# Performance work log

Hardware: AMD Instinct MI355X
Metric: run time of the kernel (lower is better)

The kernel has to match this reference:

```python
import jax, jax.numpy as jnp
import numpy as np

D_MODEL = 1024
N_HEADS = 16
HEAD_DIM = D_MODEL // N_HEADS
BLOCK_SIZE = 2048
B, T = 4, 2048


def setup_inputs() -> dict:
    key = jax.random.key(0)
    ks = jax.random.split(key, 5)
    s = 0.02
    x = jax.random.normal(ks[0], (B, T, D_MODEL), dtype=jnp.float32)
    W_qkv = jax.random.normal(ks[1], (D_MODEL, 3 * D_MODEL), dtype=jnp.float32) * s
    b_qkv = jnp.zeros((3 * D_MODEL,), dtype=jnp.float32)
    W_proj = jax.random.normal(ks[2], (D_MODEL, D_MODEL), dtype=jnp.float32) * s
    b_proj = jnp.zeros((D_MODEL,), dtype=jnp.float32)
    return {"x": x, "W_qkv": W_qkv, "b_qkv": b_qkv, "W_proj": W_proj, "b_proj": b_proj}


def reference(x, W_qkv, b_qkv, W_proj, b_proj):
    Bsz, Tlen, C = x.shape
    qkv = x @ W_qkv + b_qkv                      # [B,T,3C]
    q, k, v = jnp.split(qkv, 3, axis=2)
    # [B,T,C] -> [B,H,T,hd]
    def heads(t):
        return t.reshape(Bsz, Tlen, N_HEADS, HEAD_DIM).transpose(0, 2, 1, 3)
    q, k, v = heads(q), heads(k), heads(v)
    scale = 1.0 / jnp.sqrt(jnp.asarray(HEAD_DIM, dtype=x.dtype))
    att = jnp.einsum('bhqd,bhkd->bhqk', q, k) * scale   # [B,H,T,T]
    causal = jnp.tril(jnp.ones((Tlen, Tlen), dtype=bool))
    att = jnp.where(causal, att, jnp.asarray(-jnp.inf, dtype=att.dtype))
    att = jax.nn.softmax(att, axis=-1)
    y = jnp.einsum('bhqk,bhkd->bhqd', att, v)            # [B,H,T,hd]
    y = y.transpose(0, 2, 1, 3).reshape(Bsz, Tlen, C)
    return y @ W_proj + b_proj
```

## Files before the change

### kernel.cpp

```cpp
#include <hip/hip_runtime.h>
#include <hip/hip_bf16.h>

#define D_MODEL 1024
#define N_HEADS 16
#define HEAD_DIM 64
#define SEQ_T 2048
#define BATCH 4

#define SL2E 0.18033688011f

typedef short s8v  __attribute__((ext_vector_type(8)));
typedef float f32x4 __attribute__((ext_vector_type(4)));
typedef unsigned long long ull;

static __device__ __forceinline__ unsigned short f2bf(float f) {
  union { float f; unsigned int u; } v; v.f = f;
  unsigned int u = v.u;
  return (unsigned short)((u + 0x7FFF + ((u >> 16) & 1)) >> 16);
}

static __device__ __forceinline__ unsigned int cvtpk_bf16(float lo, float hi) {
  unsigned int r;
  asm("v_cvt_pk_bf16_f32 %0, %1, %2" : "=v"(r) : "v"(lo), "v"(hi));
  return r;
}

#if __has_builtin(__builtin_amdgcn_exp2f)
#define EXP2(x) __builtin_amdgcn_exp2f(x)
#else
#define EXP2(x) exp2f(x)
#endif

static __device__ __forceinline__ void glds16(const void* g, void* l) {
  __builtin_amdgcn_global_load_lds(
      (const __attribute__((address_space(1))) void*)g,
      (__attribute__((address_space(3))) void*)l, 16, 0, 0);
}

template<int MODE>
__global__ __launch_bounds__(256) void gemm_bt_kernel(
    const unsigned short* __restrict__ A, const unsigned short* __restrict__ Bt,
    const float* __restrict__ bias, float* __restrict__ Cout,
    unsigned short* __restrict__ qkb, unsigned short* __restrict__ vT,
    int M, int N, int K)
{
  __shared__ unsigned short Al[128 * 64];
  __shared__ unsigned short Bl[128 * 64];

  const int tid  = threadIdx.x;
  const int lane = tid & 63;
  const int wave = tid >> 6;
  const int col  = lane & 15;
  const int quad = lane >> 4;
  const int wm   = (wave & 1) * 64;
  const int wn   = (wave >> 1) * 64;
  const int bm0  = blockIdx.y * 128;
  const int bn0  = blockIdx.x * 128;
  const int cx   = col & 7;

  f32x4 acc[4][4];
  #pragma unroll
  for (int t = 0; t < 4; ++t)
    #pragma unroll
    for (int u = 0; u < 4; ++u) acc[t][u] = (f32x4)0.f;

  for (int k0 = 0; k0 < K; k0 += 64) {
    __syncthreads();
    #pragma unroll
    for (int i = 0; i < 4; ++i) {
      int idx = i * 256 + tid;
      int row = idx >> 3;
      int gc  = (idx & 7) ^ (row & 7);
      glds16(A  + (size_t)(bm0 + row) * K + k0 + gc * 8, &Al[idx * 8]);
      glds16(Bt + (size_t)(bn0 + row) * K + k0 + gc * 8, &Bl[idx * 8]);
    }
    __syncthreads();

    #pragma unroll
    for (int s = 0; s < 2; ++s) {
      s8v af[4], bf[4];
      #pragma unroll
      for (int t = 0; t < 4; ++t) {
        int ar = wm + t * 16 + col;
        af[t] = *(const s8v*)&Al[ar * 64 + (((s * 4 + quad) ^ cx) * 8)];
        int br = wn + t * 16 + col;
        bf[t] = *(const s8v*)&Bl[br * 64 + (((s * 4 + quad) ^ cx) * 8)];
      }
      #pragma unroll
      for (int t = 0; t < 4; ++t)
        #pragma unroll
        for (int u = 0; u < 4; ++u)
          acc[t][u] = __builtin_amdgcn_mfma_f32_16x16x32_bf16(
              af[t], bf[u], acc[t][u], 0, 0, 0);
    }
  }

  float bv[4];
  #pragma unroll
  for (int u = 0; u < 4; ++u) bv[u] = bias[bn0 + wn + u * 16 + col];

  if (MODE == 1 && bn0 >= 2048) {
    #pragma unroll
    for (int t = 0; t < 4; ++t) {
      int m_base = bm0 + wm + t * 16 + quad * 4;
      #pragma unroll
      for (int u = 0; u < 4; ++u) {
        int hd = (bn0 + wn + u * 16 + col) - 2048;
        size_t bh = (size_t)(bm0 >> 11) * 16 + (hd >> 6);
        ull pk = (ull)f2bf(acc[t][u][0] + bv[u])
               | ((ull)f2bf(acc[t][u][1] + bv[u]) << 16)
               | ((ull)f2bf(acc[t][u][2] + bv[u]) << 32)
               | ((ull)f2bf(acc[t][u][3] + bv[u]) << 48);
        *(ull*)(vT + (bh * 64 + (hd & 63)) * 2048 + (m_base & 2047)) = pk;
      }
    }
  } else {
    const float sc = (MODE == 1 && (bn0 + wn) < 1024) ? SL2E : 1.0f;
    #pragma unroll
    for (int t = 0; t < 4; ++t) {
      #pragma unroll
      for (int r = 0; r < 4; ++r) {
        size_t m = bm0 + wm + t * 16 + quad * 4 + r;
        #pragma unroll
        for (int u = 0; u < 4; ++u) {
          int n = bn0 + wn + u * 16 + col;
          float v = acc[t][u][r] + bv[u];
          if (MODE == 0) Cout[m * N + n] = v;
          else           qkb[m * 2048 + n] = f2bf(v * sc);
        }
      }
    }
  }
}

static __device__ __forceinline__ void transpose_tile(
    const float* __restrict__ W, unsigned short* __restrict__ Wt,
    int K, int N, int n0, int k0)
{
  __shared__ float tile[32][33];
  const int tx = threadIdx.x & 31, ty = threadIdx.x >> 5;
  #pragma unroll
  for (int i = 0; i < 4; ++i)
    tile[ty + i * 8][tx] = W[(size_t)(k0 + ty + i * 8) * N + n0 + tx];
  __syncthreads();
  #pragma unroll
  for (int i = 0; i < 4; ++i)
    Wt[(size_t)(n0 + ty + i * 8) * K + k0 + tx] = f2bf(tile[tx][ty + i * 8]);
}

__global__ __launch_bounds__(256) void prep_kernel(
    const float* __restrict__ x, const float* __restrict__ W_qkv,
    const float* __restrict__ W_proj, ushort4* __restrict__ xb,
    unsigned short* __restrict__ wqt, unsigned short* __restrict__ wpt)
{
  const int bid = blockIdx.x;
  if (bid < 8192) {
    int i = bid * 256 + threadIdx.x;
    float4 v = ((const float4*)x)[i];
    ushort4 o;
    o.x = f2bf(v.x); o.y = f2bf(v.y); o.z = f2bf(v.z); o.w = f2bf(v.w);
    xb[i] = o;
  } else if (bid < 8192 + 3072) {
    int b2 = bid - 8192;
    transpose_tile(W_qkv, wqt, 1024, 3072, (b2 % 96) * 32, (b2 / 96) * 32);
  } else {
    int b3 = bid - 11264;
    transpose_tile(W_proj, wpt, 1024, 1024, (b3 % 32) * 32, (b3 / 32) * 32);
  }
}

#define LPAD 72

__global__ __launch_bounds__(512, 4) void attn_mfma_kernel(
    const unsigned short* __restrict__ qk, const unsigned short* __restrict__ vT,
    unsigned short* __restrict__ y)
{
  __shared__ unsigned short Ks[2][64 * 64];
  __shared__ unsigned short Vs[2][64 * 64];
  __shared__ unsigned short Ps[256][LPAD];

  const int tid  = threadIdx.x;
  const int wave = tid >> 6;
  const int lane = tid & 63;
  const int col  = lane & 15;
  const int quad = lane >> 4;
  const int cx   = col & 7;

  const int bh = blockIdx.x;
  const int b = bh >> 4, h = bh & 15;
  const int yy = (int)blockIdx.y;
  const int qblk = (yy < 4) ? (7 - yy) : (yy - 4);
  const int q0 = qblk * 256;
  const int nk = 4 * qblk + 4;
  const int C2 = 2048;

  const unsigned short* qbase = qk + (size_t)b * SEQ_T * C2 + h * 64;
  const unsigned short* kbase = qbase + 1024;
  const unsigned short* vbase = vT + (size_t)bh * 64 * 2048;

  s8v qf[2][2];
  #pragma unroll
  for (int s = 0; s < 2; ++s)
    #pragma unroll
    for (int c = 0; c < 2; ++c)
      qf[s][c] = *(const s8v*)(qbase +
          (size_t)(q0 + s * 128 + wave * 16 + col) * C2 + c * 32 + quad * 8);

  f32x4 acc[2][4];
  #pragma unroll
  for (int s = 0; s < 2; ++s)
    #pragma unroll
    for (int t = 0; t < 4; ++t) acc[s][t] = (f32x4)0.f;
  float lsum[2] = {0.f, 0.f};

  auto stage = [&](int kt, int bi) {
    const int k0 = kt * 64;
    int row = tid >> 3;
    int gc  = (tid & 7) ^ (row & 7);
    glds16(kbase + (size_t)(k0 + row) * C2 + gc * 8, &Ks[bi][tid * 8]);
    glds16(vbase + (size_t)row * 2048 + k0 + gc * 8, &Vs[bi][tid * 8]);
  };

  auto tile_body = [&](int kt, int bi) {
    const int k0 = kt * 64;

    s8v kf[4][2];
    #pragma unroll
    for (int t = 0; t < 4; ++t)
      #pragma unroll
      for (int c = 0; c < 2; ++c)
        kf[t][c] = *(const s8v*)&Ks[bi][(t * 16 + col) * 64 + (((c * 4 + quad) ^ cx) * 8)];

    #pragma unroll
    for (int s = 0; s < 2; ++s) {
      const int qs = q0 + s * 128 + wave * 16;
      if (k0 > qs + 15) continue;

      f32x4 st[4];
      #pragma unroll
      for (int t = 0; t < 4; ++t) st[t] = (f32x4)0.f;
      #pragma unroll
      for (int t = 0; t < 4; ++t)
        #pragma unroll
        for (int c = 0; c < 2; ++c)
          st[t] = __builtin_amdgcn_mfma_f32_16x16x32_bf16(kf[t][c], qf[s][c], st[t], 0, 0, 0);

      const bool diag = (k0 + 63 > qs);
      if (!diag) {
        #pragma unroll
        for (int t = 0; t < 4; ++t) {
          float e0 = EXP2(st[t][0]);
          float e1 = EXP2(st[t][1]);
          float e2 = EXP2(st[t][2]);
          float e3 = EXP2(st[t][3]);
          lsum[s] += (e0 + e1) + (e2 + e3);
          uint2 pk;
          pk.x = cvtpk_bf16(e0, e1);
          pk.y = cvtpk_bf16(e2, e3);
          *(uint2*)&Ps[s * 128 + wave * 16 + col][t * 16 + quad * 4] = pk;
        }
      } else {
        const int qg = qs + col;
        #pragma unroll
        for (int t = 0; t < 4; ++t) {
          uint2 pk;
          if (k0 + t * 16 > qs + 15) {
            pk.x = 0u; pk.y = 0u;
          } else {
            float e[4];
            #pragma unroll
            for (int r = 0; r < 4; ++r) {
              float v = EXP2(st[t][r]);
              if (k0 + t * 16 + quad * 4 + r > qg) v = 0.f;
              e[r] = v;
            }
            lsum[s] += (e[0] + e[1]) + (e[2] + e[3]);
            pk.x = cvtpk_bf16(e[0], e[1]);
            pk.y = cvtpk_bf16(e[2], e[3]);
          }
          *(uint2*)&Ps[s * 128 + wave * 16 + col][t * 16 + quad * 4] = pk;
        }
      }
    }

    s8v vf[4][2];
    #pragma unroll
    for (int t = 0; t < 4; ++t)
      #pragma unroll
      for (int c = 0; c < 2; ++c)
        vf[t][c] = *(const s8v*)&Vs[bi][(t * 16 + col) * 64 + (((c * 4 + quad) ^ cx) * 8)];
    #pragma unroll
    for (int s = 0; s < 2; ++s) {
      const int qs = q0 + s * 128 + wave * 16;
      if (k0 > qs + 15) continue;
      s8v pf[2];
      #pragma unroll
      for (int c = 0; c < 2; ++c)
        pf[c] = *(const s8v*)&Ps[s * 128 + wave * 16 + col][c * 32 + quad * 8];
      #pragma unroll
      for (int t = 0; t < 4; ++t)
        #pragma unroll
        for (int c = 0; c < 2; ++c)
          acc[s][t] = __builtin_amdgcn_mfma_f32_16x16x32_bf16(pf[c], vf[t][c], acc[s][t], 0, 0, 0);
    }
  };

  stage(0, 0);
  for (int kt = 0; kt < nk; kt += 2) {
    __syncthreads();
    if (kt + 1 < nk) stage(kt + 1, 1);
    tile_body(kt, 0);
    if (kt + 1 < nk) {
      __syncthreads();
      if (kt + 2 < nk) stage(kt + 2, 0);
      tile_body(kt + 1, 1);
    }
  }

  #pragma unroll
  for (int s = 0; s < 2; ++s) {
    float v = lsum[s];
    v += __shfl_xor(v, 16);
    v += __shfl_xor(v, 32);
    #pragma unroll
    for (int r = 0; r < 4; ++r) {
      float inv = 1.0f / __shfl(v, quad * 4 + r);
      int q = q0 + s * 128 + wave * 16 + quad * 4 + r;
      unsigned short* yrow = y + (size_t)(b * SEQ_T + q) * D_MODEL + h * 64;
      #pragma unroll
      for (int t = 0; t < 4; ++t)
        yrow[t * 16 + col] = f2bf(acc[s][t][r] * inv);
    }
  }
}

extern "C" void kernel_launch(void* const* d_in, const int* in_sizes, int n_in,
                              void* d_out, int out_size, void* d_ws, size_t ws_size,
                              hipStream_t stream) {
  const float* x      = (const float*)d_in[0];
  const float* W_qkv  = (const float*)d_in[1];
  const float* b_qkv  = (const float*)d_in[2];
  const float* W_proj = (const float*)d_in[3];
  const float* b_proj = (const float*)d_in[4];
  float* out = (float*)d_out;

  const int M  = BATCH * SEQ_T;
  const int C  = D_MODEL;
  const int C3 = 3 * D_MODEL;

  unsigned short* xb  = (unsigned short*)d_ws;
  unsigned short* wqt = xb  + (size_t)M * C;
  unsigned short* wpt = wqt + (size_t)C3 * C;
  unsigned short* qkb = wpt + (size_t)C * C;
  unsigned short* vTb = qkb + (size_t)M * 2 * C;
  unsigned short* yb  = vTb + (size_t)64 * 64 * SEQ_T;

  dim3 blk(256);

  prep_kernel<<<dim3(8192 + 3072 + 1024), blk, 0, stream>>>(
      x, W_qkv, W_proj, (ushort4*)xb, wqt, wpt);

  gemm_bt_kernel<1><<<dim3(C3 / 128, M / 128), blk, 0, stream>>>(
      xb, wqt, b_qkv, nullptr, qkb, vTb, M, C3, C);

  attn_mfma_kernel<<<dim3(BATCH * N_HEADS, SEQ_T / 256), dim3(512), 0, stream>>>(
      qkb, vTb, yb);

  gemm_bt_kernel<0><<<dim3(C / 128, M / 128), blk, 0, stream>>>(
      yb, wpt, b_proj, out, nullptr, nullptr, M, C, C);
}
```

Measured before the change: 252.3 us.

## Keep softmax probabilities in registers by permuting K rows to match MFMA layout

Removes the shared-memory P staging buffer by permuting which K rows each MFMA tile reads, so the QK^T output register layout directly matches the A-operand layout of the PV MFMA. The K load swizzle is adjusted so the permuted row reads stay free of bank conflicts. This drops LDS writes and reads of P and frees LDS, at the cost of more complex index math and a changed causal-mask computation.

```diff
diff --git a/kernel.cpp b/kernel.cpp
--- a/kernel.cpp
+++ b/kernel.cpp
@@ -169,15 +169,12 @@
   }
 }
 
-#define LPAD 72
-
 __global__ __launch_bounds__(512, 4) void attn_mfma_kernel(
     const unsigned short* __restrict__ qk, const unsigned short* __restrict__ vT,
     unsigned short* __restrict__ y)
 {
   __shared__ unsigned short Ks[2][64 * 64];
   __shared__ unsigned short Vs[2][64 * 64];
-  __shared__ unsigned short Ps[256][LPAD];
 
   const int tid  = threadIdx.x;
   const int wave = tid >> 6;
@@ -216,25 +213,33 @@
   auto stage = [&](int kt, int bi) {
     const int k0 = kt * 64;
     int row = tid >> 3;
-    int gc  = (tid & 7) ^ (row & 7);
-    glds16(kbase + (size_t)(k0 + row) * C2 + gc * 8, &Ks[bi][tid * 8]);
-    glds16(vbase + (size_t)row * 2048 + k0 + gc * 8, &Vs[bi][tid * 8]);
+    int gk  = (tid & 7) ^ (row & 7) ^ ((row >> 1) & 4);
+    int gv  = (tid & 7) ^ (row & 7);
+    glds16(kbase + (size_t)(k0 + row) * C2 + gk * 8, &Ks[bi][tid * 8]);
+    glds16(vbase + (size_t)row * 2048 + k0 + gv * 8, &Vs[bi][tid * 8]);
   };
 
   auto tile_body = [&](int kt, int bi) {
     const int k0 = kt * 64;
 
     s8v kf[4][2];
-    #pragma unroll
-    for (int t = 0; t < 4; ++t)
+    const int pbase = (col >> 2) * 8 + (col & 3);
+    #pragma unroll
+    for (int t = 0; t < 4; ++t) {
+      const int rowt = pbase + (t & 1) * 4 + (t >> 1) * 32;
+      const int sx   = (rowt & 7) ^ ((rowt >> 1) & 4);
       #pragma unroll
       for (int c = 0; c < 2; ++c)
-        kf[t][c] = *(const s8v*)&Ks[bi][(t * 16 + col) * 64 + (((c * 4 + quad) ^ cx) * 8)];
-
+        kf[t][c] = *(const s8v*)&Ks[bi][rowt * 64 + (((c * 4 + quad) ^ sx) * 8)];
+    }
+
+    s8v pf[2][2];
+    bool live[2];
     #pragma unroll
     for (int s = 0; s < 2; ++s) {
       const int qs = q0 + s * 128 + wave * 16;
-      if (k0 > qs + 15) continue;
+      live[s] = (k0 <= qs + 15);
+      if (!live[s]) continue;
 
       f32x4 st[4];
       #pragma unroll
@@ -245,6 +250,7 @@
         for (int c = 0; c < 2; ++c)
           st[t] = __builtin_amdgcn_mfma_f32_16x16x32_bf16(kf[t][c], qf[s][c], st[t], 0, 0, 0);
 
+      uint2 pw[4];
       const bool diag = (k0 + 63 > qs);
       if (!diag) {
         #pragma unroll
@@ -254,32 +260,37 @@
           float e2 = EXP2(st[t][2]);
           float e3 = EXP2(st[t][3]);
           lsum[s] += (e0 + e1) + (e2 + e3);
-          uint2 pk;
-          pk.x = cvtpk_bf16(e0, e1);
-          pk.y = cvtpk_bf16(e2, e3);
-          *(uint2*)&Ps[s * 128 + wave * 16 + col][t * 16 + quad * 4] = pk;
+          pw[t].x = cvtpk_bf16(e0, e1);
+          pw[t].y = cvtpk_bf16(e2, e3);
         }
       } else {
         const int qg = qs + col;
         #pragma unroll
         for (int t = 0; t < 4; ++t) {
-          uint2 pk;
-          if (k0 + t * 16 > qs + 15) {
-            pk.x = 0u; pk.y = 0u;
+          const int kt0 = k0 + 4 * (t & 1) + 32 * (t >> 1);
+          if (kt0 > qs + 15) {
+            pw[t].x = 0u; pw[t].y = 0u;
           } else {
+            const int kq = kt0 + 8 * quad;
             float e[4];
             #pragma unroll
             for (int r = 0; r < 4; ++r) {
               float v = EXP2(st[t][r]);
-              if (k0 + t * 16 + quad * 4 + r > qg) v = 0.f;
+              if (kq + r > qg) v = 0.f;
               e[r] = v;
             }
             lsum[s] += (e[0] + e[1]) + (e[2] + e[3]);
-            pk.x = cvtpk_bf16(e[0], e[1]);
-            pk.y = cvtpk_bf16(e[2], e[3]);
+            pw[t].x = cvtpk_bf16(e[0], e[1]);
+            pw[t].y = cvtpk_bf16(e[2], e[3]);
           }
-          *(uint2*)&Ps[s * 128 + wave * 16 + col][t * 16 + quad * 4] = pk;
         }
+      }
+      #pragma unroll
+      for (int c = 0; c < 2; ++c) {
+        union { uint4 u; s8v v; } cc;
+        cc.u.x = pw[2 * c].x;  cc.u.y = pw[2 * c].y;
+        cc.u.z = pw[2 * c + 1].x;  cc.u.w = pw[2 * c + 1].y;
+        pf[s][c] = cc.v;
       }
     }
 
@@ -291,17 +302,12 @@
         vf[t][c] = *(const s8v*)&Vs[bi][(t * 16 + col) * 64 + (((c * 4 + quad) ^ cx) * 8)];
     #pragma unroll
     for (int s = 0; s < 2; ++s) {
-      const int qs = q0 + s * 128 + wave * 16;
-      if (k0 > qs + 15) continue;
-      s8v pf[2];
-      #pragma unroll
-      for (int c = 0; c < 2; ++c)
-        pf[c] = *(const s8v*)&Ps[s * 128 + wave * 16 + col][c * 32 + quad * 8];
+      if (!live[s]) continue;
       #pragma unroll
       for (int t = 0; t < 4; ++t)
         #pragma unroll
         for (int c = 0; c < 2; ++c)
-          acc[s][t] = __builtin_amdgcn_mfma_f32_16x16x32_bf16(pf[c], vf[t][c], acc[s][t], 0, 0, 0);
+          acc[s][t] = __builtin_amdgcn_mfma_f32_16x16x32_bf16(pf[s][c], vf[t][c], acc[s][t], 0, 0, 0);
     }
   };
 
```

New measurement: 238.9 us. -5.3%, faster.
